# Kernel tuning notes

Hardware: AMD Instinct MI355X
Metric: run time of the kernel (lower is better)

## Reference

```python
import jax, jax.numpy as jnp
from jax import lax
import numpy as np

BATCH = 131072
D_IN = 512
D_OUT = 512
ITERS = 10
THRES = 1e-6


def bjorck_orthonormalize(w, iters=ITERS, thres=THRES):
    """Order-1 Bjorck orthonormalization: W <- 1.5*W - 0.5*W (W^T W).

    Row-orthogonal if out<=in, column-orthogonal otherwise (operate on W^T).
    Early-stops when max|delta| <= thres, matching the module's tolerance.
    """
    transpose = w.shape[0] > w.shape[1]
    if transpose:
        w = w.T

    def cond(state):
        i, _, err = state
        return jnp.logical_and(i < iters, err > thres)

    def body(state):
        i, w, _ = state
        w_new = 1.5 * w - 0.5 * (w @ (w.T @ w))
        err = jnp.max(jnp.abs(w_new - w))
        return i + 1, w_new, err

    _, w, _ = lax.while_loop(
        cond, body, (jnp.array(0, jnp.int32), w, jnp.array(jnp.inf, w.dtype))
    )
    if transpose:
        w = w.T
    return w


def setup_inputs() -> dict:
    key = jax.random.key(0)
    k1, k2 = jax.random.split(key)
    inputs = jax.random.normal(k1, (BATCH, D_IN), dtype=jnp.float32)
    # scaled Gaussian so singular values lie in (0, sqrt(3)) -> Bjorck converges
    weight = jax.random.normal(k2, (D_OUT, D_IN), dtype=jnp.float32) * (0.5 / np.sqrt(D_IN))
    return {"inputs": inputs, "weight": weight}


def reference(inputs, weight):
    # training-mode forward with projection=True, inverse=False:
    # weight.data <- bjorck(weight.data); out = F.linear(inputs, weight)
    w_proj = bjorck_orthonormalize(weight)
    return inputs @ w_proj.T  # [batch, out_features]
```

## Files before the change

kernel.cpp:

```cpp
#include <hip/hip_runtime.h>


using bf16x8 = __attribute__((ext_vector_type(8))) short;
using f32x4  = __attribute__((ext_vector_type(4))) float;
using u16x8  = __attribute__((ext_vector_type(8))) unsigned short;

#define DI 512

__device__ __forceinline__ unsigned short f2bf(float f) {
  unsigned int u = __builtin_bit_cast(unsigned int, f);
  u += 0x7FFFu + ((u >> 16) & 1u);
  return (unsigned short)(u >> 16);
}
__device__ __forceinline__ float bf2f(unsigned short h) {
  unsigned int u = ((unsigned int)h) << 16;
  return __builtin_bit_cast(float, u);
}

__global__ void k_split(const float* __restrict__ W, float* __restrict__ Wm,
                        unsigned short* __restrict__ Wh, unsigned short* __restrict__ Wl,
                        unsigned short* __restrict__ WTh, unsigned short* __restrict__ WTl) {
  int idx = blockIdx.x * blockDim.x + threadIdx.x;
  int m = idx >> 9, i = idx & 511;
  float w = W[idx];
  Wm[idx] = w;
  unsigned short h  = f2bf(w);
  unsigned short lo = f2bf(w - bf2f(h));
  Wh[idx] = h; Wl[idx] = lo;
  WTh[i * DI + m] = h; WTl[i * DI + m] = lo;
}

__global__ __launch_bounds__(256) void k_mm2(
    const unsigned short* __restrict__ Ah, const unsigned short* __restrict__ Al,
    const unsigned short* __restrict__ Bh, const unsigned short* __restrict__ Bl,
    int mode,
    const float* __restrict__ Wm_in, float* __restrict__ Wm_out,
    unsigned short* __restrict__ Oh, unsigned short* __restrict__ Ol,
    unsigned short* __restrict__ OTh, unsigned short* __restrict__ OTl) {
  const int tid = threadIdx.x;
  const int l   = tid & 63;
  const int wid = (blockIdx.x << 2) | (tid >> 6);
  const int m0  = (wid >> 5) << 4;
  const int n0  = (wid & 31) << 4;

  const int ra = (m0 + (l & 15)) * DI + ((l >> 4) << 3);
  const int rb = (n0 + (l & 15)) * DI + ((l >> 4) << 3);

  f32x4 a0 = {}, a1 = {}, a2 = {}, a3 = {}, a4 = {}, a5 = {};
#pragma unroll
  for (int k0 = 0; k0 < DI; k0 += 64) {
    bf16x8 ah0 = *(const bf16x8*)&Ah[ra + k0];
    bf16x8 al0 = *(const bf16x8*)&Al[ra + k0];
    bf16x8 bh0 = *(const bf16x8*)&Bh[rb + k0];
    bf16x8 bl0 = *(const bf16x8*)&Bl[rb + k0];
    bf16x8 ah1 = *(const bf16x8*)&Ah[ra + k0 + 32];
    bf16x8 al1 = *(const bf16x8*)&Al[ra + k0 + 32];
    bf16x8 bh1 = *(const bf16x8*)&Bh[rb + k0 + 32];
    bf16x8 bl1 = *(const bf16x8*)&Bl[rb + k0 + 32];
    a0 = __builtin_amdgcn_mfma_f32_16x16x32_bf16(ah0, bh0, a0, 0, 0, 0);
    a1 = __builtin_amdgcn_mfma_f32_16x16x32_bf16(ah0, bl0, a1, 0, 0, 0);
    a2 = __builtin_amdgcn_mfma_f32_16x16x32_bf16(al0, bh0, a2, 0, 0, 0);
    a3 = __builtin_amdgcn_mfma_f32_16x16x32_bf16(ah1, bh1, a3, 0, 0, 0);
    a4 = __builtin_amdgcn_mfma_f32_16x16x32_bf16(ah1, bl1, a4, 0, 0, 0);
    a5 = __builtin_amdgcn_mfma_f32_16x16x32_bf16(al1, bh1, a5, 0, 0, 0);
  }
  f32x4 acc = (a0 + a1) + (a2 + a3) + (a4 + a5);

  const int r0 = m0 + ((l >> 4) << 2);
  const int cn = n0 + (l & 15);
#pragma unroll
  for (int r = 0; r < 4; ++r) {
    const int gm = r0 + r, gn = cn;
    const float v = acc[r];
    if (mode == 0) {
      unsigned short h = f2bf(v);
      Oh[gm * DI + gn] = h;
      Ol[gm * DI + gn] = f2bf(v - bf2f(h));
    } else {
      const float wn = 1.5f * Wm_in[gm * DI + gn] - 0.5f * v;
      Wm_out[gm * DI + gn] = wn;
      unsigned short h  = f2bf(wn);
      unsigned short lo = f2bf(wn - bf2f(h));
      Oh[gm * DI + gn] = h;   Ol[gm * DI + gn] = lo;
      OTh[gn * DI + gm] = h;  OTl[gn * DI + gm] = lo;
    }
  }
}

__global__ __launch_bounds__(256, 2) void k_big(
    const float* __restrict__ X, const unsigned short* __restrict__ Wp,
    float* __restrict__ out) {
  __shared__ unsigned short sX[64][40];
  __shared__ unsigned short sW[512][40];
  const int tid = threadIdx.x;
  const int w = tid >> 6, l = tid & 63;

  f32x4 acc[4][8] = {};

  const int xrow = tid >> 2, xoff = (tid & 3) << 3;
  const int wrow = tid >> 2, wchunk = (tid & 3) << 3;
  const int rowbase = blockIdx.x << 6;

  for (int k0 = 0; k0 < 512; k0 += 32) {
    __syncthreads();
    {
      const float* xp = &X[(rowbase + xrow) * 512 + k0 + xoff];
      f32x4 v0 = *(const f32x4*)xp;
      f32x4 v1 = *(const f32x4*)(xp + 4);
      u16x8 h;
      h[0] = f2bf(v0[0]); h[1] = f2bf(v0[1]); h[2] = f2bf(v0[2]); h[3] = f2bf(v0[3]);
      h[4] = f2bf(v1[0]); h[5] = f2bf(v1[1]); h[6] = f2bf(v1[2]); h[7] = f2bf(v1[3]);
      *(u16x8*)&sX[xrow][xoff] = h;
    }
#pragma unroll
    for (int p = 0; p < 8; ++p) {
      *(u16x8*)&sW[wrow + p * 64][wchunk] =
          *(const u16x8*)&Wp[(wrow + p * 64) * 512 + k0 + wchunk];
    }
    __syncthreads();
    const int ke = (l >> 4) << 3;
    bf16x8 a[4], b[8];
#pragma unroll
    for (int mf = 0; mf < 4; ++mf)
      a[mf] = *(const bf16x8*)&sX[(mf << 4) + (l & 15)][ke];
#pragma unroll
    for (int nf = 0; nf < 8; ++nf)
      b[nf] = *(const bf16x8*)&sW[(w << 7) + (nf << 4) + (l & 15)][ke];
#pragma unroll
    for (int mf = 0; mf < 4; ++mf)
#pragma unroll
      for (int nf = 0; nf < 8; ++nf)
        acc[mf][nf] = __builtin_amdgcn_mfma_f32_16x16x32_bf16(a[mf], b[nf], acc[mf][nf], 0, 0, 0);
  }

  const int cn = l & 15;
#pragma unroll
  for (int mf = 0; mf < 4; ++mf) {
    const int r0 = rowbase + (mf << 4) + ((l >> 4) << 2);
#pragma unroll
    for (int nf = 0; nf < 8; ++nf) {
      const int col = (w << 7) + (nf << 4) + cn;
#pragma unroll
      for (int r = 0; r < 4; ++r)
        out[(r0 + r) * 512 + col] = acc[mf][nf][r];
    }
  }
}

extern "C" void kernel_launch(void* const* d_in, const int* in_sizes, int n_in,
                              void* d_out, int out_size, void* d_ws, size_t ws_size,
                              hipStream_t stream) {
  const float* X = (const float*)d_in[0];
  const float* W = (const float*)d_in[1];
  float* out = (float*)d_out;

  char* ws = (char*)d_ws;
  size_t off = 0;
  auto carve = [&](size_t bytes) { void* p = ws + off; off += (bytes + 255) & ~(size_t)255; return p; };

  const size_t F32 = (size_t)DI * DI * 4;
  const size_t BF  = (size_t)DI * DI * 2;

  float* Wm[2];           unsigned short *Wh[2], *Wl[2], *WTh[2], *WTl[2];
  Wm[0]  = (float*)carve(F32);          Wm[1]  = (float*)carve(F32);
  Wh[0]  = (unsigned short*)carve(BF);  Wh[1]  = (unsigned short*)carve(BF);
  Wl[0]  = (unsigned short*)carve(BF);  Wl[1]  = (unsigned short*)carve(BF);
  WTh[0] = (unsigned short*)carve(BF);  WTh[1] = (unsigned short*)carve(BF);
  WTl[0] = (unsigned short*)carve(BF);  WTl[1] = (unsigned short*)carve(BF);
  unsigned short* Gh = (unsigned short*)carve(BF);
  unsigned short* Gl = (unsigned short*)carve(BF);

  k_split<<<1024, 256, 0, stream>>>(W, Wm[0], Wh[0], Wl[0], WTh[0], WTl[0]);

  int cur = 0;
  for (int it = 0; it < 10; ++it) {
    k_mm2<<<256, 256, 0, stream>>>(WTh[cur], WTl[cur], WTh[cur], WTl[cur], 0,
                                   nullptr, nullptr, Gh, Gl, nullptr, nullptr);
    const int nxt = cur ^ 1;
    k_mm2<<<256, 256, 0, stream>>>(Wh[cur], Wl[cur], Gh, Gl, 1,
                                   Wm[cur], Wm[nxt], Wh[nxt], Wl[nxt], WTh[nxt], WTl[nxt]);
    cur = nxt;
  }

  k_big<<<2048, 256, 0, stream>>>(X, Wh[cur], out);
}
```

Measured before the change: 369.8 us.

## Fuse Bjorck iteration matmuls into one kernel and pipeline the big GEMM

Each Bjorck iteration's two matmuls (Gram and update) are merged into a single kernel. Each block computes 16 columns of G into shared memory and then applies them to W, which removes the global G round-trip and halves the launch count. The final large GEMM now reads W fragments straight from global/L2 instead of staging them in LDS. It also double-buffers X in a swizzled LDS layout with register prefetch, swaps the MFMA operand order, and writes outputs as vectorised f32x4 stores. The fused iteration kernel runs on only 32 blocks, which may underuse the GPU, and it recomputes Gram work per block.

```diff
diff --git a/kernel.cpp b/kernel.cpp
--- a/kernel.cpp
+++ b/kernel.cpp
@@ -6,6 +6,7 @@
 using u16x8  = __attribute__((ext_vector_type(8))) unsigned short;
 
 #define DI 512
+#define GSTRIDE 528
 
 __device__ __forceinline__ unsigned short f2bf(float f) {
   unsigned int u = __builtin_bit_cast(unsigned int, f);
@@ -30,59 +31,80 @@
   WTh[i * DI + m] = h; WTl[i * DI + m] = lo;
 }
 
-__global__ __launch_bounds__(256) void k_mm2(
-    const unsigned short* __restrict__ Ah, const unsigned short* __restrict__ Al,
-    const unsigned short* __restrict__ Bh, const unsigned short* __restrict__ Bl,
-    int mode,
-    const float* __restrict__ Wm_in, float* __restrict__ Wm_out,
-    unsigned short* __restrict__ Oh, unsigned short* __restrict__ Ol,
-    unsigned short* __restrict__ OTh, unsigned short* __restrict__ OTl) {
+__global__ __launch_bounds__(512) void k_iter(
+    const unsigned short* __restrict__ WTh_c, const unsigned short* __restrict__ WTl_c,
+    const unsigned short* __restrict__ Wh_c,  const unsigned short* __restrict__ Wl_c,
+    const float* __restrict__ Wm_c,
+    float* __restrict__ Wm_n,
+    unsigned short* __restrict__ Wh_n, unsigned short* __restrict__ Wl_n,
+    unsigned short* __restrict__ WTh_n, unsigned short* __restrict__ WTl_n) {
+  __shared__ unsigned short GhT[16 * GSTRIDE];
+  __shared__ unsigned short GlT[16 * GSTRIDE];
   const int tid = threadIdx.x;
-  const int l   = tid & 63;
-  const int wid = (blockIdx.x << 2) | (tid >> 6);
-  const int m0  = (wid >> 5) << 4;
-  const int n0  = (wid & 31) << 4;
-
-  const int ra = (m0 + (l & 15)) * DI + ((l >> 4) << 3);
-  const int rb = (n0 + (l & 15)) * DI + ((l >> 4) << 3);
-
-  f32x4 a0 = {}, a1 = {}, a2 = {}, a3 = {}, a4 = {}, a5 = {};
-#pragma unroll
-  for (int k0 = 0; k0 < DI; k0 += 64) {
-    bf16x8 ah0 = *(const bf16x8*)&Ah[ra + k0];
-    bf16x8 al0 = *(const bf16x8*)&Al[ra + k0];
-    bf16x8 bh0 = *(const bf16x8*)&Bh[rb + k0];
-    bf16x8 bl0 = *(const bf16x8*)&Bl[rb + k0];
-    bf16x8 ah1 = *(const bf16x8*)&Ah[ra + k0 + 32];
-    bf16x8 al1 = *(const bf16x8*)&Al[ra + k0 + 32];
-    bf16x8 bh1 = *(const bf16x8*)&Bh[rb + k0 + 32];
-    bf16x8 bl1 = *(const bf16x8*)&Bl[rb + k0 + 32];
-    a0 = __builtin_amdgcn_mfma_f32_16x16x32_bf16(ah0, bh0, a0, 0, 0, 0);
-    a1 = __builtin_amdgcn_mfma_f32_16x16x32_bf16(ah0, bl0, a1, 0, 0, 0);
-    a2 = __builtin_amdgcn_mfma_f32_16x16x32_bf16(al0, bh0, a2, 0, 0, 0);
-    a3 = __builtin_amdgcn_mfma_f32_16x16x32_bf16(ah1, bh1, a3, 0, 0, 0);
-    a4 = __builtin_amdgcn_mfma_f32_16x16x32_bf16(ah1, bl1, a4, 0, 0, 0);
-    a5 = __builtin_amdgcn_mfma_f32_16x16x32_bf16(al1, bh1, a5, 0, 0, 0);
-  }
-  f32x4 acc = (a0 + a1) + (a2 + a3) + (a4 + a5);
-
-  const int r0 = m0 + ((l >> 4) << 2);
-  const int cn = n0 + (l & 15);
-#pragma unroll
-  for (int r = 0; r < 4; ++r) {
-    const int gm = r0 + r, gn = cn;
-    const float v = acc[r];
-    if (mode == 0) {
-      unsigned short h = f2bf(v);
-      Oh[gm * DI + gn] = h;
-      Ol[gm * DI + gn] = f2bf(v - bf2f(h));
-    } else {
-      const float wn = 1.5f * Wm_in[gm * DI + gn] - 0.5f * v;
-      Wm_out[gm * DI + gn] = wn;
-      unsigned short h  = f2bf(wn);
-      unsigned short lo = f2bf(wn - bf2f(h));
-      Oh[gm * DI + gn] = h;   Ol[gm * DI + gn] = lo;
-      OTh[gn * DI + gm] = h;  OTl[gn * DI + gm] = lo;
+  const int l = tid & 63, w = tid >> 6;
+  const int lm = l & 15, lk = l >> 4;
+  const int j = (blockIdx.x << 4) + lm;
+
+  {
+    const int rb = j * DI + (lk << 3);
+    f32x4 acc[4][3] = {};
+#pragma unroll 4
+    for (int k0 = 0; k0 < DI; k0 += 32) {
+      bf16x8 bh = *(const bf16x8*)&WTh_c[rb + k0];
+      bf16x8 bl = *(const bf16x8*)&WTl_c[rb + k0];
+#pragma unroll
+      for (int t = 0; t < 4; ++t) {
+        const int ra = ((w << 6) + (t << 4) + lm) * DI + (lk << 3) + k0;
+        bf16x8 ah = *(const bf16x8*)&WTh_c[ra];
+        bf16x8 al = *(const bf16x8*)&WTl_c[ra];
+        acc[t][0] = __builtin_amdgcn_mfma_f32_16x16x32_bf16(ah, bh, acc[t][0], 0, 0, 0);
+        acc[t][1] = __builtin_amdgcn_mfma_f32_16x16x32_bf16(ah, bl, acc[t][1], 0, 0, 0);
+        acc[t][2] = __builtin_amdgcn_mfma_f32_16x16x32_bf16(al, bh, acc[t][2], 0, 0, 0);
+      }
+    }
+#pragma unroll
+    for (int t = 0; t < 4; ++t) {
+      f32x4 v4 = (acc[t][0] + acc[t][1]) + acc[t][2];
+#pragma unroll
+      for (int r = 0; r < 4; ++r) {
+        const int i = (w << 6) + (t << 4) + (lk << 2) + r;
+        const float v = v4[r];
+        unsigned short h = f2bf(v);
+        GhT[lm * GSTRIDE + i] = h;
+        GlT[lm * GSTRIDE + i] = f2bf(v - bf2f(h));
+      }
+    }
+  }
+  __syncthreads();
+
+  {
+    f32x4 acc[4][3] = {};
+#pragma unroll 4
+    for (int k0 = 0; k0 < DI; k0 += 32) {
+      bf16x8 bh = *(const bf16x8*)&GhT[lm * GSTRIDE + k0 + (lk << 3)];
+      bf16x8 bl = *(const bf16x8*)&GlT[lm * GSTRIDE + k0 + (lk << 3)];
+#pragma unroll
+      for (int t = 0; t < 4; ++t) {
+        const int ra = ((w << 6) + (t << 4) + lm) * DI + (lk << 3) + k0;
+        bf16x8 ah = *(const bf16x8*)&Wh_c[ra];
+        bf16x8 al = *(const bf16x8*)&Wl_c[ra];
+        acc[t][0] = __builtin_amdgcn_mfma_f32_16x16x32_bf16(ah, bh, acc[t][0], 0, 0, 0);
+        acc[t][1] = __builtin_amdgcn_mfma_f32_16x16x32_bf16(ah, bl, acc[t][1], 0, 0, 0);
+        acc[t][2] = __builtin_amdgcn_mfma_f32_16x16x32_bf16(al, bh, acc[t][2], 0, 0, 0);
+      }
+    }
+#pragma unroll
+    for (int t = 0; t < 4; ++t) {
+      f32x4 v4 = (acc[t][0] + acc[t][1]) + acc[t][2];
+#pragma unroll
+      for (int r = 0; r < 4; ++r) {
+        const int m = (w << 6) + (t << 4) + (lk << 2) + r;
+        const float wn = 1.5f * Wm_c[m * DI + j] - 0.5f * v4[r];
+        Wm_n[m * DI + j] = wn;
+        unsigned short h = f2bf(wn), lo = f2bf(wn - bf2f(h));
+        Wh_n[m * DI + j] = h;   Wl_n[m * DI + j] = lo;
+        WTh_n[j * DI + m] = h;  WTl_n[j * DI + m] = lo;
+      }
     }
   }
 }
@@ -90,59 +112,71 @@
 __global__ __launch_bounds__(256, 2) void k_big(
     const float* __restrict__ X, const unsigned short* __restrict__ Wp,
     float* __restrict__ out) {
-  __shared__ unsigned short sX[64][40];
-  __shared__ unsigned short sW[512][40];
+  __shared__ unsigned short sX[2][2048];
   const int tid = threadIdx.x;
   const int w = tid >> 6, l = tid & 63;
+  const int lm = l & 15, lk = l >> 4;
+  const int ck = lk ^ ((lm >> 1) & 3);
+  const int rowbase = blockIdx.x << 6;
+
+  const int arow = tid >> 2, ac = tid & 3;
+  const int alds = (arow * 4 + (ac ^ ((arow >> 1) & 3))) * 8;
+  const float* xsrc = &X[(rowbase + arow) * DI + (ac << 3)];
 
   f32x4 acc[4][8] = {};
-
-  const int xrow = tid >> 2, xoff = (tid & 3) << 3;
-  const int wrow = tid >> 2, wchunk = (tid & 3) << 3;
-  const int rowbase = blockIdx.x << 6;
-
-  for (int k0 = 0; k0 < 512; k0 += 32) {
+  f32x4 xv[2][2];
+
+  {
+    f32x4 t0 = *(const f32x4*)xsrc;
+    f32x4 t1 = *(const f32x4*)(xsrc + 4);
+    xv[0][0] = *(const f32x4*)(xsrc + 32);
+    xv[0][1] = *(const f32x4*)(xsrc + 36);
+    xv[1][0] = *(const f32x4*)(xsrc + 64);
+    xv[1][1] = *(const f32x4*)(xsrc + 68);
+    u16x8 h;
+    h[0] = f2bf(t0[0]); h[1] = f2bf(t0[1]); h[2] = f2bf(t0[2]); h[3] = f2bf(t0[3]);
+    h[4] = f2bf(t1[0]); h[5] = f2bf(t1[1]); h[6] = f2bf(t1[2]); h[7] = f2bf(t1[3]);
+    *(u16x8*)&sX[0][alds] = h;
+  }
+  __syncthreads();
+
+#pragma unroll
+  for (int k = 0; k < 16; ++k) {
+    const int buf = k & 1;
+    if (k < 15) {
+      u16x8 h;
+      h[0] = f2bf(xv[buf][0][0]); h[1] = f2bf(xv[buf][0][1]);
+      h[2] = f2bf(xv[buf][0][2]); h[3] = f2bf(xv[buf][0][3]);
+      h[4] = f2bf(xv[buf][1][0]); h[5] = f2bf(xv[buf][1][1]);
+      h[6] = f2bf(xv[buf][1][2]); h[7] = f2bf(xv[buf][1][3]);
+      *(u16x8*)&sX[buf ^ 1][alds] = h;
+    }
+    if (k < 13) {
+      xv[buf][0] = *(const f32x4*)(xsrc + ((k + 3) << 5));
+      xv[buf][1] = *(const f32x4*)(xsrc + ((k + 3) << 5) + 4);
+    }
+    bf16x8 b[8], a[4];
+#pragma unroll
+    for (int nf = 0; nf < 8; ++nf)
+      b[nf] = *(const bf16x8*)&Wp[((w << 7) + (nf << 4) + lm) * DI + (k << 5) + (lk << 3)];
+#pragma unroll
+    for (int mf = 0; mf < 4; ++mf)
+      a[mf] = *(const bf16x8*)&sX[buf][((mf * 16 + lm) * 4 + ck) * 8];
+#pragma unroll
+    for (int mf = 0; mf < 4; ++mf)
+#pragma unroll
+      for (int nf = 0; nf < 8; ++nf)
+        acc[mf][nf] = __builtin_amdgcn_mfma_f32_16x16x32_bf16(b[nf], a[mf], acc[mf][nf], 0, 0, 0);
     __syncthreads();
-    {
-      const float* xp = &X[(rowbase + xrow) * 512 + k0 + xoff];
-      f32x4 v0 = *(const f32x4*)xp;
-      f32x4 v1 = *(const f32x4*)(xp + 4);
-      u16x8 h;
-      h[0] = f2bf(v0[0]); h[1] = f2bf(v0[1]); h[2] = f2bf(v0[2]); h[3] = f2bf(v0[3]);
-      h[4] = f2bf(v1[0]); h[5] = f2bf(v1[1]); h[6] = f2bf(v1[2]); h[7] = f2bf(v1[3]);
-      *(u16x8*)&sX[xrow][xoff] = h;
-    }
-#pragma unroll
-    for (int p = 0; p < 8; ++p) {
-      *(u16x8*)&sW[wrow + p * 64][wchunk] =
-          *(const u16x8*)&Wp[(wrow + p * 64) * 512 + k0 + wchunk];
-    }
-    __syncthreads();
-    const int ke = (l >> 4) << 3;
-    bf16x8 a[4], b[8];
-#pragma unroll
-    for (int mf = 0; mf < 4; ++mf)
-      a[mf] = *(const bf16x8*)&sX[(mf << 4) + (l & 15)][ke];
-#pragma unroll
-    for (int nf = 0; nf < 8; ++nf)
-      b[nf] = *(const bf16x8*)&sW[(w << 7) + (nf << 4) + (l & 15)][ke];
-#pragma unroll
-    for (int mf = 0; mf < 4; ++mf)
-#pragma unroll
-      for (int nf = 0; nf < 8; ++nf)
-        acc[mf][nf] = __builtin_amdgcn_mfma_f32_16x16x32_bf16(a[mf], b[nf], acc[mf][nf], 0, 0, 0);
-  }
-
-  const int cn = l & 15;
+  }
+
 #pragma unroll
   for (int mf = 0; mf < 4; ++mf) {
-    const int r0 = rowbase + (mf << 4) + ((l >> 4) << 2);
+    const int gm = rowbase + (mf << 4) + lm;
 #pragma unroll
     for (int nf = 0; nf < 8; ++nf) {
-      const int col = (w << 7) + (nf << 4) + cn;
-#pragma unroll
-      for (int r = 0; r < 4; ++r)
-        out[(r0 + r) * 512 + col] = acc[mf][nf][r];
+      const int gn = (w << 7) + (nf << 4) + (lk << 2);
+      *(f32x4*)&out[gm * DI + gn] = acc[mf][nf];
     }
   }
 }
@@ -167,18 +201,14 @@
   Wl[0]  = (unsigned short*)carve(BF);  Wl[1]  = (unsigned short*)carve(BF);
   WTh[0] = (unsigned short*)carve(BF);  WTh[1] = (unsigned short*)carve(BF);
   WTl[0] = (unsigned short*)carve(BF);  WTl[1] = (unsigned short*)carve(BF);
-  unsigned short* Gh = (unsigned short*)carve(BF);
-  unsigned short* Gl = (unsigned short*)carve(BF);
 
   k_split<<<1024, 256, 0, stream>>>(W, Wm[0], Wh[0], Wl[0], WTh[0], WTl[0]);
 
   int cur = 0;
   for (int it = 0; it < 10; ++it) {
-    k_mm2<<<256, 256, 0, stream>>>(WTh[cur], WTl[cur], WTh[cur], WTl[cur], 0,
-                                   nullptr, nullptr, Gh, Gl, nullptr, nullptr);
     const int nxt = cur ^ 1;
-    k_mm2<<<256, 256, 0, stream>>>(Wh[cur], Wl[cur], Gh, Gl, 1,
-                                   Wm[cur], Wm[nxt], Wh[nxt], Wl[nxt], WTh[nxt], WTl[nxt]);
+    k_iter<<<32, 512, 0, stream>>>(WTh[cur], WTl[cur], Wh[cur], Wl[cur], Wm[cur],
+                                   Wm[nxt], Wh[nxt], Wl[nxt], WTh[nxt], WTl[nxt]);
     cur = nxt;
   }
 
```

New measurement: 993.8 us. 2.69x slower.
